# Kernel optimization log

Measured on AMD Instinct MI355X. Metric: run time of the kernel, lower is better.

## Reference

```python
import jax, jax.numpy as jnp
import numpy as np
import math

S, B, D, H = 2048, 2, 1024, 16
HD = D // H  # head_dim = 64


def setup_inputs() -> dict:
    key = jax.random.key(0)
    ks = jax.random.split(key, 8)
    scale = 0.02
    return {
        "query": jax.random.normal(ks[0], (S, B, D), jnp.float32),
        "key": jax.random.normal(ks[1], (S, B, D), jnp.float32),
        "value": jax.random.normal(ks[2], (S, B, D), jnp.float32),
        "mask": jax.random.randint(ks[3], (1, S, 1, 1), 0, 2, jnp.int32),
        "w_q": jax.random.normal(ks[4], (D, D), jnp.float32) * scale,
        "b_q": jnp.zeros((D,), jnp.float32),
        "w_k": jax.random.normal(ks[5], (D, D), jnp.float32) * scale,
        "b_k": jnp.zeros((D,), jnp.float32),
        "w_v": jax.random.normal(ks[6], (D, D), jnp.float32) * scale,
        "b_v": jnp.zeros((D,), jnp.float32),
    }


def reference(query, key, value, mask, w_q, b_q, w_k, b_k, w_v, b_v):
    # Linear projections (torch Linear: x @ W^T + b); inputs are (S, B, D)
    q = query @ w_q.T + b_q
    k = key @ w_k.T + b_k
    v = value @ w_v.T + b_v
    # split heads: (S, B, H, HD)
    q = q.reshape(S, B, H, HD)
    k = k.reshape(S, B, H, HD)
    v = v.reshape(S, B, H, HD)
    # scores over (query_i, key_j, batch, head)
    scores = jnp.einsum("ibhd,jbhd->ijbh", q, k) * (1.0 / math.sqrt(HD))
    # mask (1, S, 1, 1) broadcasts against (i, j, b, h); 0 => masked
    scores = jnp.where(mask == 0, -jnp.inf, scores)
    # softmax over key axis j (original: nn.Softmax(dim=1))
    attn = jax.nn.softmax(scores, axis=1)
    out = jnp.einsum("ijbh,jbhd->ibhd", attn, v)  # (S, B, H, HD)
    return out.reshape(S, B, D)
```

## Files before the change

### kernel.cpp

```cpp
#include <hip/hip_runtime.h>
#include <stdint.h>


#define S_ 2048
#define B_ 2
#define D_ 1024
#define H_ 16
#define HD_ 64
#define M_ (S_ * B_)

typedef __bf16 bf16;
typedef bf16 bf16x8 __attribute__((ext_vector_type(8)));
typedef float floatx4 __attribute__((ext_vector_type(4)));

#define QSCALE 0.18033688011112042f

__device__ __forceinline__ void async_cp16(const bf16* g, bf16* l) {
    __builtin_amdgcn_global_load_lds(
        (const __attribute__((address_space(1))) void*)g,
        (__attribute__((address_space(3))) void*)l, 16, 0, 0);
}

__global__ __launch_bounds__(256) void mask_scan(const int* __restrict__ mask,
                                                 int* __restrict__ sidx,
                                                 int* __restrict__ cnt)
{
    __shared__ int sums[256];
    const int tid = threadIdx.x;
    int v[8], s = 0;
    #pragma unroll
    for (int j = 0; j < 8; j++) { v[j] = mask[tid * 8 + j] ? 1 : 0; s += v[j]; }
    sums[tid] = s;
    __syncthreads();
    for (int off = 1; off < 256; off <<= 1) {
        int t = (tid >= off) ? sums[tid - off] : 0;
        __syncthreads();
        sums[tid] += t;
        __syncthreads();
    }
    int base = (tid > 0) ? sums[tid - 1] : 0;
    #pragma unroll
    for (int j = 0; j < 8; j++)
        if (v[j]) { sidx[base] = tid * 8 + j; base++; }
    if (tid == 255) cnt[0] = sums[255];
}

__global__ __launch_bounds__(256) void cvt_gather(
    const float* __restrict__ xq, const float* __restrict__ xk, const float* __restrict__ xv,
    const int* __restrict__ sidx, const int* __restrict__ cnt,
    bf16* __restrict__ oq, bf16* __restrict__ ok, bf16* __restrict__ ov)
{
    const int z = blockIdx.y;
    const float* src = (z == 0) ? xq : (z == 1) ? xk : xv;
    bf16*        dst = (z == 0) ? oq : (z == 1) ? ok : ov;

    const int tid = threadIdx.x;
    const int rm  = blockIdx.x * 2 + (tid >> 7);
    int srow = rm;
    if (z != 0) {
        const int cs = rm >> 1, b = rm & 1;
        if (cs >= cnt[0]) return;
        srow = sidx[cs] * 2 + b;
    }
    const int col = (tid & 127) * 8;
    const floatx4* sp = (const floatx4*)(src + (size_t)srow * D_ + col);
    floatx4 x0 = sp[0], x1 = sp[1];
    bf16x8 v;
    #pragma unroll
    for (int j = 0; j < 4; j++) { v[j] = (bf16)x0[j]; v[4 + j] = (bf16)x1[j]; }
    *(bf16x8*)(dst + (size_t)rm * D_ + col) = v;
}

__global__ __launch_bounds__(256) void cvt3(
    const float* __restrict__ a, const float* __restrict__ b, const float* __restrict__ c,
    bf16* __restrict__ oa, bf16* __restrict__ ob, bf16* __restrict__ oc)
{
    const int z = blockIdx.z;
    const float* src = (z == 0) ? a : (z == 1) ? b : c;
    bf16*        dst = (z == 0) ? oa : (z == 1) ? ob : oc;
    const size_t i = ((size_t)blockIdx.x * 256 + threadIdx.x) * 8;
    floatx4 x0 = *(const floatx4*)(src + i);
    floatx4 x1 = *(const floatx4*)(src + i + 4);
    bf16x8 v;
    #pragma unroll
    for (int j = 0; j < 4; j++) { v[j] = (bf16)x0[j]; v[4 + j] = (bf16)x1[j]; }
    *(bf16x8*)(dst + i) = v;
}

#define TM 128
#define TN 128
#define BK 32

__global__ __launch_bounds__(256) void qkv_gemm_async(
    const bf16* __restrict__ xq, const bf16* __restrict__ xk, const bf16* __restrict__ xv,
    const bf16* __restrict__ wq, const bf16* __restrict__ wk, const bf16* __restrict__ wv,
    const float* __restrict__ bq, const float* __restrict__ bk, const float* __restrict__ bv,
    const int* __restrict__ cnt,
    bf16* __restrict__ oq, bf16* __restrict__ ok, bf16* __restrict__ ov)
{
    __shared__ __align__(16) bf16 a_lds[TM * BK];
    __shared__ __align__(16) bf16 b_lds[TN * BK];

    const int z = blockIdx.y;
    const bf16*  X  = (z == 0) ? xq : (z == 1) ? xk : xv;
    const bf16*  W  = (z == 0) ? wq : (z == 1) ? wk : wv;
    const float* Bi = (z == 0) ? bq : (z == 1) ? bk : bv;
    bf16*        O  = (z == 0) ? oq : (z == 1) ? ok : ov;

    const int f   = blockIdx.x;
    const int xcd = f & 7, t = f >> 3;
    const int m0  = ((t & 3) * 8 + xcd) * TM;
    const int n0  = (t >> 2) * TN;

    const int rows_active = (z == 0) ? M_ : 2 * cnt[0];
    if (m0 >= rows_active) return;

    const int tid  = threadIdx.x;
    const int wid  = tid >> 6;
    const int lane = tid & 63;
    const int wm = wid >> 1, wn = wid & 1;
    const int lm = lane & 15, lq = lane >> 4;

    const bf16* src_a = (z == 2) ? b_lds : a_lds;
    const bf16* src_b = (z == 2) ? a_lds : b_lds;
    const int a_base = ((z == 2) ? wn : wm) * 64;
    const int b_base = ((z == 2) ? wm : wn) * 64;

    floatx4 acc[4][4] = {};

    for (int kt = 0; kt < D_; kt += BK) {
        __syncthreads();
        #pragma unroll
        for (int tt = 0; tt < 2; tt++) {
            const int cb = (tt * 4 + wid) * 64;
            const int c  = cb + lane;
            const int row = c >> 2, kc = c & 3;
            async_cp16(X + (size_t)(m0 + row) * D_ + kt + kc * 8, a_lds + cb * 8);
            async_cp16(W + (size_t)(n0 + row) * D_ + kt + kc * 8, b_lds + cb * 8);
        }
        __syncthreads();

        bf16x8 af[4], bfv[4];
        #pragma unroll
        for (int i = 0; i < 4; i++)
            af[i] = *(const bf16x8*)(src_a + (a_base + i * 16 + lm) * BK + lq * 8);
        #pragma unroll
        for (int j = 0; j < 4; j++)
            bfv[j] = *(const bf16x8*)(src_b + (b_base + j * 16 + lm) * BK + lq * 8);
        #pragma unroll
        for (int i = 0; i < 4; i++)
            #pragma unroll
            for (int j = 0; j < 4; j++)
                acc[i][j] = __builtin_amdgcn_mfma_f32_16x16x32_bf16(
                    af[i], bfv[j], acc[i][j], 0, 0, 0);
    }

    if (z != 2) {
        #pragma unroll
        for (int j = 0; j < 4; j++) {
            const int n = n0 + wn * 64 + j * 16 + lm;
            const float bias = Bi[n];
            const int h = n >> 6, hd = n & 63;
            #pragma unroll
            for (int i = 0; i < 4; i++) {
                const int mb = m0 + wm * 64 + i * 16 + lq * 4;
                #pragma unroll
                for (int r = 0; r < 4; r++) {
                    const int m = mb + r;
                    const int row = m >> 1, b = m & 1;
                    float v = acc[i][j][r] + bias;
                    if (z == 0) v *= QSCALE;
                    O[(((size_t)(b * H_ + h)) * S_ + row) * HD_ + hd] = (bf16)v;
                }
            }
        }
    } else {
        #pragma unroll
        for (int j = 0; j < 4; j++) {
            const int m = m0 + wm * 64 + j * 16 + lm;
            const int cs = m >> 1, b = m & 1;
            #pragma unroll
            for (int i = 0; i < 4; i++) {
                const int wb = n0 + wn * 64 + i * 16 + lq * 4;
                #pragma unroll
                for (int r = 0; r < 4; r++) {
                    const int n = wb + r;
                    const float bias = Bi[n];
                    const int h = n >> 6, d = n & 63;
                    O[(((size_t)(b * H_ + h)) * HD_ + d) * S_ + cs] =
                        (bf16)(acc[i][j][r] + bias);
                }
            }
        }
    }
}

#define KT 64
#define QB 128

__global__ __launch_bounds__(256) void attn_kernel(
    const bf16* __restrict__ qw, const bf16* __restrict__ kw, const bf16* __restrict__ vtw,
    const int* __restrict__ cnt, float* __restrict__ out)
{
    __shared__ __align__(16) bf16 k_lds[2 * KT * HD_];
    __shared__ __align__(16) bf16 v_ldsT[2 * HD_ * KT];
    __shared__ __align__(16) bf16 p_lds[4 * 2 * 16 * 72];

    const int tid  = threadIdx.x;
    const int wid  = tid >> 6;
    const int lane = tid & 63;
    const int lm = lane & 15, lq = lane >> 4;
    const int bh = blockIdx.y;
    const int q0 = blockIdx.x * QB;
    const int count = cnt[0];

    const bf16* Qb  = qw  + (size_t)bh * S_ * HD_;
    const bf16* Kb  = kw  + (size_t)bh * S_ * HD_;
    const bf16* VTb = vtw + (size_t)bh * HD_ * S_;

    bf16x8 qf[2][2];
    #pragma unroll
    for (int t = 0; t < 2; t++) {
        const bf16* qp = Qb + (size_t)(q0 + wid * 32 + t * 16 + lm) * HD_;
        qf[t][0] = *(const bf16x8*)(qp + lq * 8);
        qf[t][1] = *(const bf16x8*)(qp + 32 + lq * 8);
    }

    float lsum[2][4] = {};
    floatx4 oacc[2][4] = {};
    bf16* pwb = p_lds + wid * (2 * 16 * 72);

    const int c0row = tid >> 3, c0ch = tid & 7;
    const int c1row = (tid + 256) >> 3, c1ch = tid & 7;

    {
        bf16x8 kv0 = *(const bf16x8*)(Kb + (size_t)c0row * HD_ + c0ch * 8);
        bf16x8 kv1 = *(const bf16x8*)(Kb + (size_t)c1row * HD_ + c1ch * 8);
        bf16x8 vv0 = *(const bf16x8*)(VTb + (size_t)c0row * S_ + c0ch * 8);
        bf16x8 vv1 = *(const bf16x8*)(VTb + (size_t)c1row * S_ + c1ch * 8);
        *(bf16x8*)(k_lds + c0row * 64 + ((c0ch ^ (c0row & 7)) * 8)) = kv0;
        *(bf16x8*)(k_lds + c1row * 64 + ((c1ch ^ (c1row & 7)) * 8)) = kv1;
        *(bf16x8*)(v_ldsT + c0row * 64 + ((c0ch ^ (c0row & 7)) * 8)) = vv0;
        *(bf16x8*)(v_ldsT + c1row * 64 + ((c1ch ^ (c1row & 7)) * 8)) = vv1;
    }
    __syncthreads();

    const int nt = (count + KT - 1) / KT;
    for (int it = 0; it < nt; ++it) {
        const int j0  = it * KT;
        const int cur = it & 1, nxt = cur ^ 1;
        const bool has_next = (it + 1 < nt);
        const bf16* kc = k_lds + cur * (KT * 64);
        const bf16* vc = v_ldsT + cur * (KT * 64);

        bf16x8 kreg0, kreg1, vreg0, vreg1;
        if (has_next) {
            const int jn = j0 + KT;
            kreg0 = *(const bf16x8*)(Kb + (size_t)(jn + c0row) * HD_ + c0ch * 8);
            kreg1 = *(const bf16x8*)(Kb + (size_t)(jn + c1row) * HD_ + c1ch * 8);
            vreg0 = *(const bf16x8*)(VTb + (size_t)c0row * S_ + jn + c0ch * 8);
            vreg1 = *(const bf16x8*)(VTb + (size_t)c1row * S_ + jn + c1ch * 8);
        }

        floatx4 sacc[2][4] = {};
        __builtin_amdgcn_s_setprio(1);
        #pragma unroll
        for (int ks = 0; ks < 2; ks++)
            #pragma unroll
            for (int n = 0; n < 4; n++) {
                bf16x8 kf = *(const bf16x8*)(kc + (n * 16 + lm) * 64 +
                                             (((ks * 4 + lq) ^ (lm & 7)) * 8));
                sacc[0][n] = __builtin_amdgcn_mfma_f32_16x16x32_bf16(qf[0][ks], kf, sacc[0][n], 0, 0, 0);
                sacc[1][n] = __builtin_amdgcn_mfma_f32_16x16x32_bf16(qf[1][ks], kf, sacc[1][n], 0, 0, 0);
            }
        __builtin_amdgcn_s_setprio(0);

        bool valid[4];
        #pragma unroll
        for (int n = 0; n < 4; n++)
            valid[n] = (j0 + n * 16 + lm < count);

        #pragma unroll
        for (int t = 0; t < 2; t++)
            #pragma unroll
            for (int r = 0; r < 4; r++)
                #pragma unroll
                for (int n = 0; n < 4; n++) {
                    const float p = valid[n] ? exp2f(sacc[t][n][r]) : 0.0f;
                    lsum[t][r] += p;
                    pwb[t * (16 * 72) + (lq * 4 + r) * 72 + n * 16 + lm] = (bf16)p;
                }

        asm volatile("s_waitcnt lgkmcnt(0)" ::: "memory");
        __builtin_amdgcn_sched_barrier(0);

        __builtin_amdgcn_s_setprio(1);
        #pragma unroll
        for (int ks = 0; ks < 2; ks++) {
            bf16x8 pf0 = *(const bf16x8*)(pwb + lm * 72 + ks * 32 + lq * 8);
            bf16x8 pf1 = *(const bf16x8*)(pwb + (16 * 72) + lm * 72 + ks * 32 + lq * 8);
            #pragma unroll
            for (int n = 0; n < 4; n++) {
                bf16x8 vf = *(const bf16x8*)(vc + (n * 16 + lm) * 64 +
                                             (((ks * 4 + lq) ^ (lm & 7)) * 8));
                oacc[0][n] = __builtin_amdgcn_mfma_f32_16x16x32_bf16(pf0, vf, oacc[0][n], 0, 0, 0);
                oacc[1][n] = __builtin_amdgcn_mfma_f32_16x16x32_bf16(pf1, vf, oacc[1][n], 0, 0, 0);
            }
        }
        __builtin_amdgcn_s_setprio(0);

        if (has_next) {
            bf16* kd = k_lds + nxt * (KT * 64);
            bf16* vd = v_ldsT + nxt * (KT * 64);
            *(bf16x8*)(kd + c0row * 64 + ((c0ch ^ (c0row & 7)) * 8)) = kreg0;
            *(bf16x8*)(kd + c1row * 64 + ((c1ch ^ (c1row & 7)) * 8)) = kreg1;
            *(bf16x8*)(vd + c0row * 64 + ((c0ch ^ (c0row & 7)) * 8)) = vreg0;
            *(bf16x8*)(vd + c1row * 64 + ((c1ch ^ (c1row & 7)) * 8)) = vreg1;
        }
        __syncthreads();
    }

    float invl[2][4];
    #pragma unroll
    for (int t = 0; t < 2; t++)
        #pragma unroll
        for (int r = 0; r < 4; r++) {
            float lr = lsum[t][r];
            lr += __shfl_xor(lr, 1);
            lr += __shfl_xor(lr, 2);
            lr += __shfl_xor(lr, 4);
            lr += __shfl_xor(lr, 8);
            invl[t][r] = 1.0f / lr;
        }
    const int b = bh >> 4, h = bh & 15;
    #pragma unroll
    for (int t = 0; t < 2; t++)
        #pragma unroll
        for (int n = 0; n < 4; n++)
            #pragma unroll
            for (int r = 0; r < 4; r++) {
                const int q = q0 + wid * 32 + t * 16 + lq * 4 + r;
                out[((size_t)q * B_ + b) * D_ + h * 64 + n * 16 + lm] =
                    oacc[t][n][r] * invl[t][r];
            }
}

extern "C" void kernel_launch(void* const* d_in, const int* in_sizes, int n_in,
                              void* d_out, int out_size, void* d_ws, size_t ws_size,
                              hipStream_t stream) {
    const float* xq = (const float*)d_in[0];
    const float* xk = (const float*)d_in[1];
    const float* xv = (const float*)d_in[2];
    const int*  mask = (const int*)d_in[3];
    const float* wq = (const float*)d_in[4];
    const float* bq = (const float*)d_in[5];
    const float* wk = (const float*)d_in[6];
    const float* bk = (const float*)d_in[7];
    const float* wv = (const float*)d_in[8];
    const float* bv = (const float*)d_in[9];

    const size_t NX = (size_t)M_ * D_;
    const size_t NW = (size_t)D_ * D_;
    char* ws = (char*)d_ws;
    int* cnt  = (int*)ws;
    int* sidx = cnt + 16;
    char* base = ws + 16384;

    bf16* xqb = (bf16*)base;
    bf16* xkb = xqb + NX;
    bf16* xvb = xkb + NX;
    bf16* wqb = xvb + NX;
    bf16* wkb = wqb + NW;
    bf16* wvb = wkb + NW;
    bf16* q_ws  = wvb + NW;
    bf16* k_ws  = q_ws + NX;
    bf16* vt_ws = k_ws + NX;

    mask_scan<<<1, 256, 0, stream>>>(mask, sidx, cnt);
    cvt_gather<<<dim3(M_ / 2, 3), 256, 0, stream>>>(xq, xk, xv, sidx, cnt,
                                                    xqb, xkb, xvb);
    cvt3<<<dim3(NW / 2048, 1, 3), 256, 0, stream>>>(wq, wk, wv, wqb, wkb, wvb);

    qkv_gemm_async<<<dim3(256, 3), 256, 0, stream>>>(xqb, xkb, xvb, wqb, wkb, wvb,
                                                     bq, bk, bv, cnt,
                                                     q_ws, k_ws, vt_ws);

    attn_kernel<<<dim3(S_ / QB, B_ * H_), 256, 0, stream>>>(q_ws, k_ws, vt_ws,
                                                            cnt, (float*)d_out);
}
```

Baseline: 206.7 us.

## Double-buffer QKV GEMM LDS tiles with XOR swizzle and MFMA priority

Doubles the LDS tile buffers in the QKV projection GEMM so the next K-slice's async global-to-LDS copies are issued before the MFMAs on the current slice run, which overlaps load latency with compute. The loop now needs one barrier per iteration instead of two. It also XOR-swizzles the 16-byte chunk placement within each row to cut LDS bank conflicts on fragment reads, and raises wave priority around the MFMA block. The cost is twice the LDS footprint (32 KB), which may lower occupancy, and a full vmcnt(0) drain each iteration that limits how much latency is actually hidden.

```diff
diff --git a/kernel.cpp b/kernel.cpp
--- a/kernel.cpp
+++ b/kernel.cpp
@@ -98,8 +98,8 @@
     const int* __restrict__ cnt,
     bf16* __restrict__ oq, bf16* __restrict__ ok, bf16* __restrict__ ov)
 {
-    __shared__ __align__(16) bf16 a_lds[TM * BK];
-    __shared__ __align__(16) bf16 b_lds[TN * BK];
+    __shared__ __align__(16) bf16 a_lds[2][TM * BK];
+    __shared__ __align__(16) bf16 b_lds[2][TN * BK];
 
     const int z = blockIdx.y;
     const bf16*  X  = (z == 0) ? xq : (z == 1) ? xk : xv;
@@ -121,39 +121,68 @@
     const int wm = wid >> 1, wn = wid & 1;
     const int lm = lane & 15, lq = lane >> 4;
 
-    const bf16* src_a = (z == 2) ? b_lds : a_lds;
-    const bf16* src_b = (z == 2) ? a_lds : b_lds;
     const int a_base = ((z == 2) ? wn : wm) * 64;
     const int b_base = ((z == 2) ? wm : wn) * 64;
 
     floatx4 acc[4][4] = {};
 
-    for (int kt = 0; kt < D_; kt += BK) {
-        __syncthreads();
-        #pragma unroll
-        for (int tt = 0; tt < 2; tt++) {
-            const int cb = (tt * 4 + wid) * 64;
-            const int c  = cb + lane;
-            const int row = c >> 2, kc = c & 3;
-            async_cp16(X + (size_t)(m0 + row) * D_ + kt + kc * 8, a_lds + cb * 8);
-            async_cp16(W + (size_t)(n0 + row) * D_ + kt + kc * 8, b_lds + cb * 8);
-        }
-        __syncthreads();
+    #define GEMM_STAGE(buf, kt)                                                 \
+        {                                                                       \
+            _Pragma("unroll")                                                   \
+            for (int tt = 0; tt < 2; tt++) {                                    \
+                const int cb  = (tt * 4 + wid) * 64;                            \
+                const int c   = cb + lane;                                      \
+                const int row = c >> 2;                                         \
+                const int kcs = (c & 3) ^ ((c >> 3) & 3);                       \
+                async_cp16(X + (size_t)(m0 + row) * D_ + (kt) + kcs * 8,        \
+                           a_lds[buf] + cb * 8);                                \
+                async_cp16(W + (size_t)(n0 + row) * D_ + (kt) + kcs * 8,        \
+                           b_lds[buf] + cb * 8);                                \
+            }                                                                   \
+        }
+
+    #define GEMM_DRAIN_BARRIER()                                                \
+        {                                                                       \
+            asm volatile("s_waitcnt vmcnt(0)" ::: "memory");                    \
+            __builtin_amdgcn_sched_barrier(0);                                  \
+            __syncthreads();                                                    \
+        }
+
+    GEMM_STAGE(0, 0);
+    GEMM_DRAIN_BARRIER();
+
+    const int nk = D_ / BK;
+    for (int ki = 0; ki < nk; ki++) {
+        const int cur = ki & 1;
+        if (ki + 1 < nk) GEMM_STAGE(cur ^ 1, (ki + 1) * BK);
+
+        const bf16* src_a = (z == 2) ? b_lds[cur] : a_lds[cur];
+        const bf16* src_b = (z == 2) ? a_lds[cur] : b_lds[cur];
 
         bf16x8 af[4], bfv[4];
         #pragma unroll
-        for (int i = 0; i < 4; i++)
-            af[i] = *(const bf16x8*)(src_a + (a_base + i * 16 + lm) * BK + lq * 8);
-        #pragma unroll
-        for (int j = 0; j < 4; j++)
-            bfv[j] = *(const bf16x8*)(src_b + (b_base + j * 16 + lm) * BK + lq * 8);
+        for (int i = 0; i < 4; i++) {
+            const int r = a_base + i * 16 + lm;
+            af[i] = *(const bf16x8*)(src_a + r * BK + ((lq ^ ((r >> 1) & 3)) * 8));
+        }
+        #pragma unroll
+        for (int j = 0; j < 4; j++) {
+            const int r = b_base + j * 16 + lm;
+            bfv[j] = *(const bf16x8*)(src_b + r * BK + ((lq ^ ((r >> 1) & 3)) * 8));
+        }
+        __builtin_amdgcn_s_setprio(1);
         #pragma unroll
         for (int i = 0; i < 4; i++)
             #pragma unroll
             for (int j = 0; j < 4; j++)
                 acc[i][j] = __builtin_amdgcn_mfma_f32_16x16x32_bf16(
                     af[i], bfv[j], acc[i][j], 0, 0, 0);
-    }
+        __builtin_amdgcn_s_setprio(0);
+
+        GEMM_DRAIN_BARRIER();
+    }
+    #undef GEMM_STAGE
+    #undef GEMM_DRAIN_BARRIER
 
     if (z != 2) {
         #pragma unroll
```

After: 219.2 us. 6.0% more time.
